# Optimization experiments

Hardware: AMD Instinct MI355X
Metric: run time of the kernel (lower is better)

Reference implementation:

```python
import jax, jax.numpy as jnp
import numpy as np

N_SRC = 2_000_000   # coords at feat_depth (fine level)
N_TGT = 1_000_000   # coords at feat_depth-1 (coarse level)
E = 8_000_000       # neighbor edges from get_neighbours
C = 32              # feature channels


def setup_inputs() -> dict:
    key = jax.random.key(0)
    k1, k2, k3, k4 = jax.random.split(key, 4)
    feat = jax.random.normal(k1, (N_SRC, C), dtype=jnp.float32)
    src_ids = jax.random.randint(k2, (E,), 0, N_SRC)
    tgt_ids = jax.random.randint(k3, (E,), 0, N_TGT)
    ntypes = jax.random.randint(k4, (E, 3), -1, 27).astype(jnp.int32)
    return {"feat": feat, "src_ids": src_ids, "tgt_ids": tgt_ids,
            "ntypes": ntypes, "n_tgt": N_TGT}


def reference(feat, src_ids, tgt_ids, ntypes, n_tgt):
    # p_masks = torch.all(ntypes >= 0, dim=1)
    p_mask = jnp.all(ntypes >= 0, axis=1)                  # [E] bool
    # Route masked-out edges to a dummy segment (index n_tgt) instead of
    # boolean-filtering, keeping shapes static for jit.
    seg = jnp.where(p_mask, tgt_ids, n_tgt)                # [E]
    gathered = feat[src_ids]                               # [E, C] irregular gather
    sums = jax.ops.segment_sum(gathered, seg, num_segments=n_tgt + 1)[:n_tgt]
    counts = jax.ops.segment_sum(jnp.ones((seg.shape[0],), feat.dtype), seg,
                                 num_segments=n_tgt + 1)[:n_tgt]
    # scatter_mean: empty segments yield 0 (torch_scatter semantics)
    out = jnp.where(counts[:, None] > 0, sums / jnp.maximum(counts[:, None], 1), 0.0)
    return out  # feat_depth - 1 is a trivial python int, omitted
```

## Files before the change

### kernel.cpp

```cpp
#include <hip/hip_runtime.h>


#define CCH 32
#define BSH 10
#define BKT 1024
#define CAP 14336
#define BIN_TILE 8192
typedef unsigned int u32;
typedef float f32x4 __attribute__((ext_vector_type(4)));

__global__ __launch_bounds__(256) void init_bcur_kernel(u32* __restrict__ bcur,
                                                        int NB) {
  int i = blockIdx.x * 256 + threadIdx.x;
  if (i < NB) bcur[i] = (u32)i * (u32)CAP;
}

__global__ __launch_bounds__(1024) void bin_fixed_kernel(
    const int* __restrict__ src_ids, const int* __restrict__ tgt_ids,
    const int* __restrict__ ntypes, u32* __restrict__ bcur,
    u32* __restrict__ pairs, int E, int NB) {
  __shared__ unsigned short s_b[BIN_TILE];
  __shared__ u32 s_pw[BIN_TILE];
  __shared__ u32 s_cnt[2048];
  __shared__ u32 s_base[2048];
  const long long base = (long long)blockIdx.x * BIN_TILE;

  for (int j = threadIdx.x; j < 2048; j += 1024) s_cnt[j] = 0;
  __syncthreads();

  for (int k = 0; k < BIN_TILE / 1024; ++k) {
    const int i = threadIdx.x + k * 1024;
    const long long e = base + i;
    unsigned short bb = 0xFFFFu;
    u32 pw = 0;
    if (e < E) {
      const long long eb = 3LL * e;
      const int n0 = __builtin_nontemporal_load(&ntypes[eb]);
      const int n1 = __builtin_nontemporal_load(&ntypes[eb + 1]);
      const int n2 = __builtin_nontemporal_load(&ntypes[eb + 2]);
      if ((n0 | n1 | n2) >= 0) {
        const u32 t = (u32)__builtin_nontemporal_load(&tgt_ids[e]);
        const u32 s = (u32)__builtin_nontemporal_load(&src_ids[e]);
        bb = (unsigned short)(t >> BSH);
        pw = (s << BSH) | (t & (BKT - 1u));
        atomicAdd(&s_cnt[bb], 1u);
      }
    }
    s_b[i] = bb;
    s_pw[i] = pw;
  }
  __syncthreads();

  for (int j = threadIdx.x; j < NB; j += 1024) {
    const u32 c = s_cnt[j];
    s_base[j] = c ? atomicAdd(&bcur[j], c) : 0u;
    s_cnt[j] = 0;
  }
  __syncthreads();

  for (int k = 0; k < BIN_TILE / 1024; ++k) {
    const int i = threadIdx.x + k * 1024;
    const unsigned short bb = s_b[i];
    if (bb != 0xFFFFu) {
      const u32 loc = atomicAdd(&s_cnt[bb], 1u);
      const u32 slot = s_base[bb] + loc;
      if (slot < ((u32)bb + 1u) * (u32)CAP) pairs[slot] = s_pw[i];
    }
  }
}

__global__ __launch_bounds__(1024) void csr_build_kernel(
    u32* __restrict__ pairs, const u32* __restrict__ bcur,
    u32* __restrict__ offsets, int n_tgt) {
  __shared__ u32 s_pw[CAP];
  __shared__ u32 s_cnt[BKT];
  __shared__ u32 s_off[BKT];
  const int b = blockIdx.x;
  const u32 wbeg = (u32)b * (u32)CAP;
  u32 fill = bcur[b] - wbeg;
  if (fill > (u32)CAP) fill = (u32)CAP;

  for (u32 i = threadIdx.x; i < fill; i += 1024) s_pw[i] = pairs[wbeg + i];
  s_cnt[threadIdx.x] = 0;
  __syncthreads();
  for (u32 i = threadIdx.x; i < fill; i += 1024)
    atomicAdd(&s_cnt[s_pw[i] & (BKT - 1u)], 1u);
  __syncthreads();

  const u32 v = s_cnt[threadIdx.x];
  s_off[threadIdx.x] = v;
  __syncthreads();
  for (int d = 1; d < BKT; d <<= 1) {
    const u32 add = (threadIdx.x >= (unsigned)d) ? s_off[threadIdx.x - d] : 0u;
    __syncthreads();
    s_off[threadIdx.x] += add;
    __syncthreads();
  }
  const u32 excl = s_off[threadIdx.x] - v;

  const int t0 = b << BSH;
  if (t0 + (int)threadIdx.x < n_tgt)
    offsets[t0 + threadIdx.x] = (v << 16) | excl;

  s_cnt[threadIdx.x] = excl;
  __syncthreads();
  for (u32 i = threadIdx.x; i < fill; i += 1024) {
    const u32 pw = s_pw[i];
    const u32 loc = atomicAdd(&s_cnt[pw & (BKT - 1u)], 1u);
    pairs[wbeg + loc] = pw >> BSH;
  }
}

__global__ __launch_bounds__(256) void gather_reduce_kernel(
    const float* __restrict__ feat, const u32* __restrict__ csr,
    const u32* __restrict__ offsets, float* __restrict__ out, int n_tgt) {
  const int tid = blockIdx.x * 256 + threadIdx.x;
  const int t = tid >> 3;
  const int g = tid & 7;
  if (t >= n_tgt) return;
  const u32 off = __builtin_nontemporal_load(&offsets[t]);
  const u32 n = off >> 16;
  const u32 base = ((u32)(t >> BSH)) * (u32)CAP + (off & 0xFFFFu);
  const int l4 = g * 4;

  f32x4 acc = {0.f, 0.f, 0.f, 0.f};
  for (u32 c = 0; c < n; c += 8) {
    const u32 m = n - c;
    u32 idx[8];
#pragma unroll
    for (int k = 0; k < 8; ++k)
      idx[k] = __builtin_nontemporal_load(
          &csr[base + c + ((u32)k < m ? (u32)k : 0u)]);
    f32x4 v[8];
#pragma unroll
    for (int k = 0; k < 8; ++k)
      v[k] = *reinterpret_cast<const f32x4*>(feat +
                                             (long long)idx[k] * CCH + l4);
#pragma unroll
    for (int k = 0; k < 8; ++k) {
      const float w = ((u32)k < m) ? 1.0f : 0.0f;
      acc += v[k] * w;
    }
  }
  const float inv = n ? 1.0f / (float)n : 0.0f;
  const f32x4 r = acc * inv;
  __builtin_nontemporal_store(
      r, reinterpret_cast<f32x4*>(out + (long long)t * CCH + l4));
}


__global__ __launch_bounds__(256) void scatter_accum_kernel(
    const float* __restrict__ feat, const int* __restrict__ src_ids,
    const int* __restrict__ tgt_ids, const int* __restrict__ ntypes,
    float* __restrict__ sums, u32* __restrict__ counts,
    long long total_threads) {
  long long tid = (long long)blockIdx.x * blockDim.x + threadIdx.x;
  if (tid >= total_threads) return;
  const int e = (int)(tid >> 3);
  const int g = (int)(tid & 7);
  const long long eb = 3LL * e;
  if ((ntypes[eb] | ntypes[eb + 1] | ntypes[eb + 2]) < 0) return;
  const int s = src_ids[e];
  const int t = tgt_ids[e];
  const float4 v =
      *reinterpret_cast<const float4*>(feat + (long long)s * CCH + g * 4);
  float* dst = sums + (long long)t * CCH + g * 4;
  atomicAdd(dst + 0, v.x);
  atomicAdd(dst + 1, v.y);
  atomicAdd(dst + 2, v.z);
  atomicAdd(dst + 3, v.w);
  if (g == 0) atomicAdd(counts + t, 1u);
}

__global__ __launch_bounds__(256) void finalize_kernel(
    float* __restrict__ out, const u32* __restrict__ counts, int total_vec4) {
  int tid = blockIdx.x * blockDim.x + threadIdx.x;
  if (tid >= total_vec4) return;
  const int t = tid >> 3;
  const u32 cnt = counts[t];
  float4* p = reinterpret_cast<float4*>(out) + tid;
  float4 v = *p;
  const float inv = (cnt > 0u) ? (1.0f / (float)cnt) : 0.0f;
  v.x *= inv; v.y *= inv; v.z *= inv; v.w *= inv;
  *p = v;
}


extern "C" void kernel_launch(void* const* d_in, const int* in_sizes, int n_in,
                              void* d_out, int out_size, void* d_ws,
                              size_t ws_size, hipStream_t stream) {
  const float* feat    = (const float*)d_in[0];
  const int*   src_ids = (const int*)d_in[1];
  const int*   tgt_ids = (const int*)d_in[2];
  const int*   ntypes  = (const int*)d_in[3];
  const int E     = in_sizes[1];
  const int n_src = in_sizes[0] / CCH;
  const int n_tgt = out_size / CCH;

  const int NB = (n_tgt + BKT - 1) >> BSH;

  const size_t need =
      ((size_t)NB * CAP + NB + (size_t)n_tgt) * sizeof(u32);
  const bool shapes_ok =
      NB <= 2048 && n_src <= (1 << 22) &&
      (long long)E <= (long long)NB * CAP * 3 / 4;

  if (ws_size >= need && shapes_ok) {
    u32* pairs   = (u32*)d_ws;
    u32* bcur    = pairs + (size_t)NB * CAP;
    u32* offsets = bcur + NB;

    init_bcur_kernel<<<(NB + 255) / 256, 256, 0, stream>>>(bcur, NB);
    const int bblocks = (E + BIN_TILE - 1) / BIN_TILE;
    bin_fixed_kernel<<<bblocks, 1024, 0, stream>>>(src_ids, tgt_ids, ntypes,
                                                   bcur, pairs, E, NB);
    csr_build_kernel<<<NB, 1024, 0, stream>>>(pairs, bcur, offsets, n_tgt);
    const long long gthreads = (long long)n_tgt * 8;
    const int gblocks = (int)((gthreads + 255) / 256);
    gather_reduce_kernel<<<gblocks, 256, 0, stream>>>(feat, pairs, offsets,
                                                      (float*)d_out, n_tgt);
  } else {
    float* sums   = (float*)d_out;
    u32*   counts = (u32*)d_ws;
    hipMemsetAsync(d_out, 0, (size_t)out_size * sizeof(float), stream);
    hipMemsetAsync(d_ws, 0, (size_t)n_tgt * sizeof(u32), stream);
    const long long total_threads = (long long)E * 8;
    const long long nblocks = (total_threads + 255) / 256;
    scatter_accum_kernel<<<(dim3)((unsigned int)nblocks), 256, 0, stream>>>(
        feat, src_ids, tgt_ids, ntypes, sums, counts, total_threads);
    const int total_vec4 = n_tgt * 8;
    finalize_kernel<<<(total_vec4 + 255) / 256, 256, 0, stream>>>(
        sums, counts, total_vec4);
  }
}
```

Baseline: 294.6 us.

## Fuse CSR build and gather-reduce into one per-bucket kernel using LDS

Merges the per-bucket counting sort and the gather-mean into a single kernel that keeps the sorted source indices in shared memory. This removes the global write-back of sorted indices, the offsets array and one launch. CAP shrinks so that both LDS arrays fit, which lowers headroom for buckets that overflow. Only 977 blocks of 1024 threads now run the gather phase, which may limit parallelism and latency hiding.

```diff
diff --git a/kernel.cpp b/kernel.cpp
--- a/kernel.cpp
+++ b/kernel.cpp
@@ -4,7 +4,7 @@
 #define CCH 32
 #define BSH 10
 #define BKT 1024
-#define CAP 14336
+#define CAP 8960
 #define BIN_TILE 8192
 typedef unsigned int u32;
 typedef float f32x4 __attribute__((ext_vector_type(4)));
@@ -69,10 +69,11 @@
   }
 }
 
-__global__ __launch_bounds__(1024) void csr_build_kernel(
-    u32* __restrict__ pairs, const u32* __restrict__ bcur,
-    u32* __restrict__ offsets, int n_tgt) {
+__global__ __launch_bounds__(1024, 8) void sort_gather_kernel(
+    const float* __restrict__ feat, const u32* __restrict__ pairs,
+    const u32* __restrict__ bcur, float* __restrict__ out, int n_tgt) {
   __shared__ u32 s_pw[CAP];
+  __shared__ u32 s_srt[CAP];
   __shared__ u32 s_cnt[BKT];
   __shared__ u32 s_off[BKT];
   const int b = blockIdx.x;
@@ -80,7 +81,8 @@
   u32 fill = bcur[b] - wbeg;
   if (fill > (u32)CAP) fill = (u32)CAP;
 
-  for (u32 i = threadIdx.x; i < fill; i += 1024) s_pw[i] = pairs[wbeg + i];
+  for (u32 i = threadIdx.x; i < fill; i += 1024)
+    s_pw[i] = __builtin_nontemporal_load(&pairs[wbeg + i]);
   s_cnt[threadIdx.x] = 0;
   __syncthreads();
   for (u32 i = threadIdx.x; i < fill; i += 1024)
@@ -96,56 +98,46 @@
     s_off[threadIdx.x] += add;
     __syncthreads();
   }
-  const u32 excl = s_off[threadIdx.x] - v;
-
-  const int t0 = b << BSH;
-  if (t0 + (int)threadIdx.x < n_tgt)
-    offsets[t0 + threadIdx.x] = (v << 16) | excl;
-
-  s_cnt[threadIdx.x] = excl;
+  s_cnt[threadIdx.x] = s_off[threadIdx.x] - v;
   __syncthreads();
   for (u32 i = threadIdx.x; i < fill; i += 1024) {
     const u32 pw = s_pw[i];
     const u32 loc = atomicAdd(&s_cnt[pw & (BKT - 1u)], 1u);
-    pairs[wbeg + loc] = pw >> BSH;
-  }
-}
-
-__global__ __launch_bounds__(256) void gather_reduce_kernel(
-    const float* __restrict__ feat, const u32* __restrict__ csr,
-    const u32* __restrict__ offsets, float* __restrict__ out, int n_tgt) {
-  const int tid = blockIdx.x * 256 + threadIdx.x;
-  const int t = tid >> 3;
-  const int g = tid & 7;
-  if (t >= n_tgt) return;
-  const u32 off = __builtin_nontemporal_load(&offsets[t]);
-  const u32 n = off >> 16;
-  const u32 base = ((u32)(t >> BSH)) * (u32)CAP + (off & 0xFFFFu);
-  const int l4 = g * 4;
-
-  f32x4 acc = {0.f, 0.f, 0.f, 0.f};
-  for (u32 c = 0; c < n; c += 8) {
-    const u32 m = n - c;
-    u32 idx[8];
+    s_srt[loc] = pw >> BSH;
+  }
+  __syncthreads();
+
+  const int grp = threadIdx.x >> 3;
+  const int lane = threadIdx.x & 7;
+  const int l4 = lane * 4;
+  const long long t0 = (long long)b << BSH;
+  for (int r = grp; r < BKT; r += 128) {
+    const long long t = t0 + r;
+    if (t >= n_tgt) break;
+    const u32 beg = r ? s_off[r - 1] : 0u;
+    const u32 n = s_off[r] - beg;
+    f32x4 acc = {0.f, 0.f, 0.f, 0.f};
+    for (u32 c = 0; c < n; c += 8) {
+      const u32 m = n - c;
+      u32 idx[8];
 #pragma unroll
-    for (int k = 0; k < 8; ++k)
-      idx[k] = __builtin_nontemporal_load(
-          &csr[base + c + ((u32)k < m ? (u32)k : 0u)]);
-    f32x4 v[8];
+      for (int k = 0; k < 8; ++k)
+        idx[k] = s_srt[beg + c + ((u32)k < m ? (u32)k : 0u)];
+      f32x4 vv[8];
 #pragma unroll
-    for (int k = 0; k < 8; ++k)
-      v[k] = *reinterpret_cast<const f32x4*>(feat +
-                                             (long long)idx[k] * CCH + l4);
+      for (int k = 0; k < 8; ++k)
+        vv[k] = *reinterpret_cast<const f32x4*>(feat +
+                                                (long long)idx[k] * CCH + l4);
 #pragma unroll
-    for (int k = 0; k < 8; ++k) {
-      const float w = ((u32)k < m) ? 1.0f : 0.0f;
-      acc += v[k] * w;
+      for (int k = 0; k < 8; ++k) {
+        const float w = ((u32)k < m) ? 1.0f : 0.0f;
+        acc += vv[k] * w;
+      }
     }
-  }
-  const float inv = n ? 1.0f / (float)n : 0.0f;
-  const f32x4 r = acc * inv;
-  __builtin_nontemporal_store(
-      r, reinterpret_cast<f32x4*>(out + (long long)t * CCH + l4));
+    const float inv = n ? 1.0f / (float)n : 0.0f;
+    acc *= inv;
+    *reinterpret_cast<f32x4*>(out + t * CCH + l4) = acc;
+  }
 }
 
 
@@ -199,26 +191,21 @@
 
   const int NB = (n_tgt + BKT - 1) >> BSH;
 
-  const size_t need =
-      ((size_t)NB * CAP + NB + (size_t)n_tgt) * sizeof(u32);
+  const size_t need = ((size_t)NB * CAP + NB) * sizeof(u32);
+  const long long mean_fill = ((long long)E * BKT + n_tgt - 1) / n_tgt;
   const bool shapes_ok =
-      NB <= 2048 && n_src <= (1 << 22) &&
-      (long long)E <= (long long)NB * CAP * 3 / 4;
+      NB <= 2048 && n_src <= (1 << 21) && mean_fill <= 8192;
 
   if (ws_size >= need && shapes_ok) {
-    u32* pairs   = (u32*)d_ws;
-    u32* bcur    = pairs + (size_t)NB * CAP;
-    u32* offsets = bcur + NB;
+    u32* pairs = (u32*)d_ws;
+    u32* bcur  = pairs + (size_t)NB * CAP;
 
     init_bcur_kernel<<<(NB + 255) / 256, 256, 0, stream>>>(bcur, NB);
     const int bblocks = (E + BIN_TILE - 1) / BIN_TILE;
     bin_fixed_kernel<<<bblocks, 1024, 0, stream>>>(src_ids, tgt_ids, ntypes,
                                                    bcur, pairs, E, NB);
-    csr_build_kernel<<<NB, 1024, 0, stream>>>(pairs, bcur, offsets, n_tgt);
-    const long long gthreads = (long long)n_tgt * 8;
-    const int gblocks = (int)((gthreads + 255) / 256);
-    gather_reduce_kernel<<<gblocks, 256, 0, stream>>>(feat, pairs, offsets,
-                                                      (float*)d_out, n_tgt);
+    sort_gather_kernel<<<NB, 1024, 0, stream>>>(feat, pairs, bcur,
+                                                (float*)d_out, n_tgt);
   } else {
     float* sums   = (float*)d_out;
     u32*   counts = (u32*)d_ws;
```

Result: faster. 268.6 us (-8.8%).
